# Kernel tuning notes

Measured on AMD Instinct MI355X. Metric: run time of the kernel, lower is better.

## Reference

```python
import jax, jax.numpy as jnp
import numpy as np

NUM_EMBEDDINGS = 8192
EMBEDDING_DIM = 256
COMMITMENT_COST = 0.25


def setup_inputs() -> dict:
    key = jax.random.key(0)
    k1, k2 = jax.random.split(key)
    x = jax.random.normal(k1, (8, 4096, EMBEDDING_DIM), dtype=jnp.float32)
    # torch init: uniform(-1/K, 1/K)
    codebook = jax.random.uniform(
        k2, (NUM_EMBEDDINGS, EMBEDDING_DIM), dtype=jnp.float32,
        minval=-1.0 / NUM_EMBEDDINGS, maxval=1.0 / NUM_EMBEDDINGS)
    return {"x": x, "codebook": codebook}


def reference(x, codebook):
    D = codebook.shape[1]
    K = codebook.shape[0]
    flat_x = x.reshape(-1, D)                      # [N, D]
    distances = (jnp.sum(flat_x * flat_x, axis=1, keepdims=True)
                 + jnp.sum(codebook * codebook, axis=1)
                 - 2.0 * jnp.matmul(flat_x, codebook.T))
    encoding_indices = jnp.argmin(distances, axis=1)  # [N]
    # direct gather instead of one-hot matmul (same math)
    quantized = codebook[encoding_indices].reshape(x.shape)

    sg = jax.lax.stop_gradient
    e_latent_loss = jnp.mean((sg(quantized) - x) ** 2)
    q_latent_loss = jnp.mean((quantized - sg(x)) ** 2)
    loss = q_latent_loss + COMMITMENT_COST * e_latent_loss

    quantized_st = x + sg(quantized - x)

    # avg one-hot probs via counts
    counts = jnp.bincount(encoding_indices, length=K)
    avg_probs = counts.astype(x.dtype) / encoding_indices.shape[0]
    perplexity = jnp.exp(-jnp.sum(avg_probs * jnp.log(avg_probs + 1e-10)))
    return quantized_st, loss, perplexity
```

## Files before the change

kernel.cpp:

```cpp
#include <hip/hip_runtime.h>
#include <cfloat>
#include <math.h>

#define NUM_EMB 8192
#define DIM 256
#define NROWS 32768
#define NSPLIT 4
#define CHUNKS 16

typedef float f32x4 __attribute__((ext_vector_type(4)));
typedef int   i32x4 __attribute__((ext_vector_type(4)));
typedef int   i32x8 __attribute__((ext_vector_type(8)));

#define GL2LDS(g, l) __builtin_amdgcn_global_load_lds( \
    (const __attribute__((address_space(1))) void*)(g), \
    (__attribute__((address_space(3))) void*)(l), 16, 0, 0)

__global__ __launch_bounds__(256) void vq_prep(const float* __restrict__ x,
                                               unsigned char* __restrict__ xq,
                                               const float* __restrict__ cb,
                                               unsigned char* __restrict__ cbq,
                                               float* __restrict__ cbn,
                                               unsigned int* __restrict__ counts) {
    int b = blockIdx.x;
    if (b < 4096) {
        int i = b * 256 + threadIdx.x;
        float4 v0 = ((const float4*)x)[2 * i];
        float4 v1 = ((const float4*)x)[2 * i + 1];
        int p0 = __builtin_amdgcn_cvt_pk_fp8_f32(v0.x, v0.y, 0, false);
        p0     = __builtin_amdgcn_cvt_pk_fp8_f32(v0.z, v0.w, p0, true);
        int p1 = __builtin_amdgcn_cvt_pk_fp8_f32(v1.x, v1.y, 0, false);
        p1     = __builtin_amdgcn_cvt_pk_fp8_f32(v1.z, v1.w, p1, true);
        ((int2*)xq)[i] = make_int2(p0, p1);
    } else if (b < 6144) {
        int row  = (b - 4096) * 4 + (threadIdx.x >> 6);
        int lane = threadIdx.x & 63;
        float4 v = ((const float4*)(cb + (size_t)row * DIM))[lane];
        int p = __builtin_amdgcn_cvt_pk_fp8_f32(v.x * 8192.f, v.y * 8192.f, 0, false);
        p     = __builtin_amdgcn_cvt_pk_fp8_f32(v.z * 8192.f, v.w * 8192.f, p, true);
        ((int*)cbq)[row * 64 + lane] = p;
        float s = v.x * v.x + v.y * v.y + v.z * v.z + v.w * v.w;
        #pragma unroll
        for (int off = 32; off > 0; off >>= 1) s += __shfl_down(s, off, 64);
        if (lane == 0) cbn[row] = 8192.f * s + 512.f;
    } else {
        counts[(b - 6144) * 256 + threadIdx.x] = 0u;
    }
}

__global__ __launch_bounds__(256, 4) void vq_argmin_mfma(
        const unsigned char* __restrict__ xq,
        const unsigned char* __restrict__ cbq,
        const float* __restrict__ cbn,
        unsigned long long* __restrict__ partial) {
    __shared__ __align__(16) unsigned char Bs[128 * 256];
    __shared__ unsigned long long redk[2][64];

    const int tid = threadIdx.x;
    const int lane = tid & 63;
    const int w = tid >> 6;
    const int wm = w >> 1, wn = w & 1;
    const int l15 = lane & 15, q = lane >> 4;
    const int ns = blockIdx.x & (NSPLIT - 1);
    const int by = blockIdx.x / NSPLIT;
    const int m0 = by * 64;
    const int nbase = ns * (NUM_EMB / NSPLIT);

    i32x8 afr[2][2];
    #pragma unroll
    for (int kc = 0; kc < 2; kc++)
        #pragma unroll
        for (int i = 0; i < 2; i++) {
            const unsigned char* p =
                xq + (size_t)(m0 + wm * 32 + i * 16 + l15) * 256 + kc * 128 + q * 32;
            i32x4 lo = *(const i32x4*)p;
            i32x4 hi = *(const i32x4*)(p + 16);
            afr[kc][i] = __builtin_shufflevector(lo, hi, 0, 1, 2, 3, 4, 5, 6, 7);
        }

    unsigned int colb[4];
    #pragma unroll
    for (int j = 0; j < 4; j++) colb[j] = (unsigned)(wn * 64 + j * 16 + l15);

    unsigned int runk[2][4];
    #pragma unroll
    for (int i = 0; i < 2; i++)
        #pragma unroll
        for (int r = 0; r < 4; r++) runk[i][r] = 0xFFFFFFFFu;

    const int sr = lane >> 4;
    const int sv = lane & 15;

    #pragma unroll 1
    for (int ch = 0; ch < CHUNKS; ch++) {
        const int n0c = nbase + ch * 128;
        const unsigned int chb = (unsigned)ch << 7;
        unsigned int cj[4];
        float bnj[4];
        #pragma unroll
        for (int j = 0; j < 4; j++) {
            cj[j] = chb | colb[j];
            bnj[j] = cbn[n0c + (int)colb[j]];
        }

        f32x4 acc[2][4];
        #pragma unroll
        for (int i = 0; i < 2; i++)
            #pragma unroll
            for (int j = 0; j < 4; j++) acc[i][j] = (f32x4)0.f;

        __syncthreads();
        #pragma unroll
        for (int t = 0; t < 8; t++) {
            int s = t * 4 + w;
            int row = s * 4 + sr;
            int kcs = sv >> 3, blk = sv & 7;
            GL2LDS(cbq + (size_t)(n0c + row) * 256 + kcs * 128 + ((blk ^ (row & 7)) * 16),
                   (char*)Bs + s * 1024);
        }
        __syncthreads();

        #pragma unroll
        for (int kc = 0; kc < 2; kc++) {
            #pragma unroll
            for (int j = 0; j < 4; j++) {
                int row = wn * 64 + j * 16 + l15;
                int base = row * 256 + kc * 128;
                int s0 = ((2 * q) ^ (row & 7)) * 16;
                int s1 = ((2 * q + 1) ^ (row & 7)) * 16;
                i32x4 lo = *(const i32x4*)(Bs + base + s0);
                i32x4 hi = *(const i32x4*)(Bs + base + s1);
                i32x8 bfr = __builtin_shufflevector(lo, hi, 0, 1, 2, 3, 4, 5, 6, 7);
                acc[0][j] = __builtin_amdgcn_mfma_scale_f32_16x16x128_f8f6f4(
                    afr[kc][0], bfr, acc[0][j], 0, 0, 0, 127, 0, 127);
                acc[1][j] = __builtin_amdgcn_mfma_scale_f32_16x16x128_f8f6f4(
                    afr[kc][1], bfr, acc[1][j], 0, 0, 0, 127, 0, 127);
            }
        }

        #pragma unroll
        for (int i = 0; i < 2; i++) {
            #pragma unroll
            for (int r = 0; r < 4; r++) {
                unsigned int k0 = (__float_as_uint(fmaf(-2.f, acc[i][0][r], bnj[0])) & 0xFFFFF800u) | cj[0];
                unsigned int k1 = (__float_as_uint(fmaf(-2.f, acc[i][1][r], bnj[1])) & 0xFFFFF800u) | cj[1];
                unsigned int k2 = (__float_as_uint(fmaf(-2.f, acc[i][2][r], bnj[2])) & 0xFFFFF800u) | cj[2];
                unsigned int k3 = (__float_as_uint(fmaf(-2.f, acc[i][3][r], bnj[3])) & 0xFFFFF800u) | cj[3];
                runk[i][r] = min(runk[i][r], min(min(k0, k1), min(k2, k3)));
            }
        }
    }

    #pragma unroll
    for (int i = 0; i < 2; i++) {
        #pragma unroll
        for (int r = 0; r < 4; r++) {
            unsigned int rk = runk[i][r];
            unsigned int gcol = (unsigned)nbase + (rk & 0x7FFu);
            unsigned long long key =
                ((unsigned long long)(rk & 0xFFFFF800u) << 32) | gcol;
            #pragma unroll
            for (int off = 8; off >= 1; off >>= 1) {
                unsigned long long o = __shfl_xor(key, off, 16);
                if (o < key) key = o;
            }
            if (l15 == 0) redk[wn][wm * 32 + i * 16 + q * 4 + r] = key;
        }
    }
    __syncthreads();
    if (tid < 64) {
        unsigned long long k0 = redk[0][tid], k1 = redk[1][tid];
        partial[(size_t)ns * NROWS + m0 + tid] = k0 < k1 ? k0 : k1;
    }
}

__global__ __launch_bounds__(256) void vq_out(const float* __restrict__ x,
                                              const float* __restrict__ cb,
                                              const unsigned long long* __restrict__ partial,
                                              float* __restrict__ out,
                                              unsigned int* __restrict__ counts,
                                              double* __restrict__ loss_part) {
    __shared__ float wred[4];
    int wv   = threadIdx.x >> 6;
    int row  = blockIdx.x * 4 + wv;
    int lane = threadIdx.x & 63;
    unsigned long long k = 0xFFFFFFFFFFFFFFFFull;
    #pragma unroll
    for (int t = 0; t < NSPLIT; t++) {
        unsigned long long v = partial[(size_t)t * NROWS + row];
        if (v < k) k = v;
    }
    int id = (int)(unsigned int)(k & 0xffffffffu);
    float4 qv = ((const float4*)(cb + (size_t)id * DIM))[lane];
    float4 xv = ((const float4*)(x + (size_t)row * DIM))[lane];
    float dx = qv.x - xv.x, dy = qv.y - xv.y, dz = qv.z - xv.z, dw = qv.w - xv.w;
    float4 o;
    o.x = xv.x + dx; o.y = xv.y + dy; o.z = xv.z + dz; o.w = xv.w + dw;
    ((float4*)(out + (size_t)row * DIM))[lane] = o;
    float s = dx * dx + dy * dy + dz * dz + dw * dw;
    #pragma unroll
    for (int o2 = 32; o2 > 0; o2 >>= 1) s += __shfl_down(s, o2, 64);
    if (lane == 0) {
        wred[wv] = s;
        atomicAdd(&counts[id], 1u);
    }
    __syncthreads();
    if (threadIdx.x == 0) {
        loss_part[blockIdx.x] =
            (double)wred[0] + (double)wred[1] + (double)wred[2] + (double)wred[3];
    }
}

__global__ __launch_bounds__(256) void vq_fin(const unsigned int* __restrict__ counts,
                                              const double* __restrict__ loss_part,
                                              float* __restrict__ out_tail) {
    __shared__ double sh[256];
    __shared__ double sl[256];
    int tid = threadIdx.x;
    double h = 0.0;
    for (int k = tid; k < NUM_EMB; k += 256) {
        float p = (float)counts[k] / 32768.0f;
        h += (double)p * log((double)p + 1e-10);
    }
    double ls = 0.0;
    for (int b = tid; b < NROWS / 4; b += 256) ls += loss_part[b];
    sh[tid] = h;
    sl[tid] = ls;
    __syncthreads();
    for (int o = 128; o > 0; o >>= 1) {
        if (tid < o) { sh[tid] += sh[tid + o]; sl[tid] += sl[tid + o]; }
        __syncthreads();
    }
    if (tid == 0) {
        double mean = sl[0] / (double)((size_t)NROWS * DIM);
        out_tail[0] = (float)(1.25 * mean);
        out_tail[1] = (float)exp(-sh[0]);
    }
}

extern "C" void kernel_launch(void* const* d_in, const int* in_sizes, int n_in,
                              void* d_out, int out_size, void* d_ws, size_t ws_size,
                              hipStream_t stream) {
    const float* x  = (const float*)d_in[0];
    const float* cb = (const float*)d_in[1];
    char* ws = (char*)d_ws;
    unsigned int* counts   = (unsigned int*)(ws + 256);
    float* cbn             = (float*)(ws + 33024);
    unsigned char* xq      = (unsigned char*)(ws + 65792);
    unsigned char* cbq     = (unsigned char*)(ws + 65792 + 8388608);
    unsigned long long* pp = (unsigned long long*)(ws + 65792 + 8388608 + 2097152);
    double* loss_part      = (double*)(ws + 65792 + 8388608 + 2097152 + 16777216);
    float* out = (float*)d_out;

    vq_prep       <<<6176, 256, 0, stream>>>(x, xq, cb, cbq, cbn, counts);
    vq_argmin_mfma<<<512 * NSPLIT, 256, 0, stream>>>(xq, cbq, cbn, pp);
    vq_out        <<<8192, 256, 0, stream>>>(x, cb, pp, out, counts, loss_part);
    vq_fin        <<<1, 256, 0, stream>>>(counts, loss_part, out + (size_t)NROWS * DIM);
}
```

Measured before the change: 208.4 us.

## Double-buffer codebook tiles, fold norms into MFMA accumulator, fuse finalize kernel

The argmin kernel now uses 64-column chunks with two LDS buffers, so the next chunk's global-to-LDS loads are issued while the current chunk is computed, and only one barrier is needed per chunk. The input x is negated and the codebook norms are halved, so the MFMA accumulator starts from the norm and the per-element fma is dropped. The separate single-block finalize kernel is folded into vq_out through a last-block ticket counter, removing one launch. This adds atomics and fences for the ticket, and the fast __logf changes entropy precision slightly.

```diff
diff --git a/kernel.cpp b/kernel.cpp
--- a/kernel.cpp
+++ b/kernel.cpp
@@ -6,7 +6,7 @@
 #define DIM 256
 #define NROWS 32768
 #define NSPLIT 4
-#define CHUNKS 16
+#define CHUNKS 32
 
 typedef float f32x4 __attribute__((ext_vector_type(4)));
 typedef int   i32x4 __attribute__((ext_vector_type(4)));
@@ -15,22 +15,26 @@
 #define GL2LDS(g, l) __builtin_amdgcn_global_load_lds( \
     (const __attribute__((address_space(1))) void*)(g), \
     (__attribute__((address_space(3))) void*)(l), 16, 0, 0)
+
+#define MFMA(A, B, C) __builtin_amdgcn_mfma_scale_f32_16x16x128_f8f6f4( \
+    (A), (B), (C), 0, 0, 0, 127, 0, 127)
 
 __global__ __launch_bounds__(256) void vq_prep(const float* __restrict__ x,
                                                unsigned char* __restrict__ xq,
                                                const float* __restrict__ cb,
                                                unsigned char* __restrict__ cbq,
                                                float* __restrict__ cbn,
-                                               unsigned int* __restrict__ counts) {
+                                               unsigned int* __restrict__ counts,
+                                               unsigned int* __restrict__ syncc) {
     int b = blockIdx.x;
     if (b < 4096) {
         int i = b * 256 + threadIdx.x;
         float4 v0 = ((const float4*)x)[2 * i];
         float4 v1 = ((const float4*)x)[2 * i + 1];
-        int p0 = __builtin_amdgcn_cvt_pk_fp8_f32(v0.x, v0.y, 0, false);
-        p0     = __builtin_amdgcn_cvt_pk_fp8_f32(v0.z, v0.w, p0, true);
-        int p1 = __builtin_amdgcn_cvt_pk_fp8_f32(v1.x, v1.y, 0, false);
-        p1     = __builtin_amdgcn_cvt_pk_fp8_f32(v1.z, v1.w, p1, true);
+        int p0 = __builtin_amdgcn_cvt_pk_fp8_f32(-v0.x, -v0.y, 0, false);
+        p0     = __builtin_amdgcn_cvt_pk_fp8_f32(-v0.z, -v0.w, p0, true);
+        int p1 = __builtin_amdgcn_cvt_pk_fp8_f32(-v1.x, -v1.y, 0, false);
+        p1     = __builtin_amdgcn_cvt_pk_fp8_f32(-v1.z, -v1.w, p1, true);
         ((int2*)xq)[i] = make_int2(p0, p1);
     } else if (b < 6144) {
         int row  = (b - 4096) * 4 + (threadIdx.x >> 6);
@@ -42,9 +46,10 @@
         float s = v.x * v.x + v.y * v.y + v.z * v.z + v.w * v.w;
         #pragma unroll
         for (int off = 32; off > 0; off >>= 1) s += __shfl_down(s, off, 64);
-        if (lane == 0) cbn[row] = 8192.f * s + 512.f;
+        if (lane == 0) cbn[row] = 4096.f * s + 256.f;
     } else {
         counts[(b - 6144) * 256 + threadIdx.x] = 0u;
+        if (b == 6144 && threadIdx.x == 0) *syncc = 0u;
     }
 }
 
@@ -53,7 +58,7 @@
         const unsigned char* __restrict__ cbq,
         const float* __restrict__ cbn,
         unsigned long long* __restrict__ partial) {
-    __shared__ __align__(16) unsigned char Bs[128 * 256];
+    __shared__ __align__(16) unsigned char Bs[2][16384];
     __shared__ unsigned long long redk[2][64];
 
     const int tid = threadIdx.x;
@@ -62,25 +67,31 @@
     const int wm = w >> 1, wn = w & 1;
     const int l15 = lane & 15, q = lane >> 4;
     const int ns = blockIdx.x & (NSPLIT - 1);
-    const int by = blockIdx.x / NSPLIT;
+    const int by = blockIdx.x >> 2;
     const int m0 = by * 64;
     const int nbase = ns * (NUM_EMB / NSPLIT);
 
-    i32x8 afr[2][2];
-    #pragma unroll
-    for (int kc = 0; kc < 2; kc++)
-        #pragma unroll
-        for (int i = 0; i < 2; i++) {
-            const unsigned char* p =
-                xq + (size_t)(m0 + wm * 32 + i * 16 + l15) * 256 + kc * 128 + q * 32;
-            i32x4 lo = *(const i32x4*)p;
-            i32x4 hi = *(const i32x4*)(p + 16);
-            afr[kc][i] = __builtin_shufflevector(lo, hi, 0, 1, 2, 3, 4, 5, 6, 7);
-        }
-
-    unsigned int colb[4];
-    #pragma unroll
-    for (int j = 0; j < 4; j++) colb[j] = (unsigned)(wn * 64 + j * 16 + l15);
+    i32x8 afr00, afr01, afr10, afr11;
+    {
+        const unsigned char* p = xq + (size_t)(m0 + wm * 32 + l15) * 256 + q * 32;
+        i32x4 lo, hi;
+        lo = *(const i32x4*)(p);                  hi = *(const i32x4*)(p + 16);
+        afr00 = __builtin_shufflevector(lo, hi, 0, 1, 2, 3, 4, 5, 6, 7);
+        lo = *(const i32x4*)(p + 16 * 256);       hi = *(const i32x4*)(p + 16 * 256 + 16);
+        afr01 = __builtin_shufflevector(lo, hi, 0, 1, 2, 3, 4, 5, 6, 7);
+        lo = *(const i32x4*)(p + 128);            hi = *(const i32x4*)(p + 128 + 16);
+        afr10 = __builtin_shufflevector(lo, hi, 0, 1, 2, 3, 4, 5, 6, 7);
+        lo = *(const i32x4*)(p + 16 * 256 + 128); hi = *(const i32x4*)(p + 16 * 256 + 128 + 16);
+        afr11 = __builtin_shufflevector(lo, hi, 0, 1, 2, 3, 4, 5, 6, 7);
+    }
+
+    const int row0 = wn * 32 + l15;
+    const int sw = row0 & 7;
+    const int vA = row0 * 256 + (((2 * q) ^ sw) * 16);
+    const int vB = row0 * 256 + (((2 * q + 1) ^ sw) * 16);
+
+    const unsigned int colb0 = (unsigned)(wn * 32 + l15);
+    const unsigned int colb1 = colb0 + 16;
 
     unsigned int runk[2][4];
     #pragma unroll
@@ -90,65 +101,74 @@
 
     const int sr = lane >> 4;
     const int sv = lane & 15;
+    const int kcs = sv >> 3, blk = sv & 7;
+    const unsigned char* gs[4];
+    int sg[4];
+    #pragma unroll
+    for (int t = 0; t < 4; t++) {
+        int s = t * 4 + w;
+        int r = s * 4 + sr;
+        gs[t] = cbq + (size_t)(nbase + r) * 256 + (size_t)(kcs * 128 + ((blk ^ (r & 7)) * 16));
+        sg[t] = s * 1024;
+    }
+
+    #pragma unroll
+    for (int t = 0; t < 4; t++) GL2LDS(gs[t], (char*)&Bs[0][0] + sg[t]);
+    #pragma unroll
+    for (int t = 0; t < 4; t++) gs[t] += 16384;
+    const float* bnp = cbn + nbase;
+    float bn0 = bnp[colb0];
+    float bn1 = bnp[colb1];
+    __syncthreads();
+
+#define BLOAD(CUR, OFF) ({ \
+    i32x4 lo_ = *(const i32x4*)(&Bs[CUR][0] + vA + (OFF)); \
+    i32x4 hi_ = *(const i32x4*)(&Bs[CUR][0] + vB + (OFF)); \
+    __builtin_shufflevector(lo_, hi_, 0, 1, 2, 3, 4, 5, 6, 7); })
+
+#define CHUNK_BODY(CHV, CUR, NXT, LAST) do { \
+    float nbn0 = bnp[64 + (int)colb0]; \
+    float nbn1 = bnp[64 + (int)colb1]; \
+    if (!(LAST)) { \
+        GL2LDS(gs[0], (char*)&Bs[NXT][0] + sg[0]); \
+        GL2LDS(gs[1], (char*)&Bs[NXT][0] + sg[1]); \
+        GL2LDS(gs[2], (char*)&Bs[NXT][0] + sg[2]); \
+        GL2LDS(gs[3], (char*)&Bs[NXT][0] + sg[3]); \
+    } \
+    gs[0] += 16384; gs[1] += 16384; gs[2] += 16384; gs[3] += 16384; \
+    f32x4 ci0; ci0[0] = bn0; ci0[1] = bn0; ci0[2] = bn0; ci0[3] = bn0; \
+    f32x4 ci1; ci1[0] = bn1; ci1[1] = bn1; ci1[2] = bn1; ci1[3] = bn1; \
+    i32x8 b_ = BLOAD(CUR, 0); \
+    f32x4 a00 = MFMA(afr00, b_, ci0); \
+    f32x4 a10 = MFMA(afr01, b_, ci0); \
+    b_ = BLOAD(CUR, 128); \
+    a00 = MFMA(afr10, b_, a00); \
+    a10 = MFMA(afr11, b_, a10); \
+    b_ = BLOAD(CUR, 4096); \
+    f32x4 a01 = MFMA(afr00, b_, ci1); \
+    f32x4 a11 = MFMA(afr01, b_, ci1); \
+    b_ = BLOAD(CUR, 4224); \
+    a01 = MFMA(afr10, b_, a01); \
+    a11 = MFMA(afr11, b_, a11); \
+    unsigned int chb = ((unsigned)(CHV)) << 6; \
+    unsigned int cj0 = chb | colb0, cj1 = chb | colb1; \
+    _Pragma("unroll") \
+    for (int r = 0; r < 4; r++) { \
+        unsigned int k00 = (__float_as_uint(a00[r]) & 0xFFFFF800u) | cj0; \
+        unsigned int k01 = (__float_as_uint(a01[r]) & 0xFFFFF800u) | cj1; \
+        runk[0][r] = min(min(k00, k01), runk[0][r]); \
+        unsigned int k10 = (__float_as_uint(a10[r]) & 0xFFFFF800u) | cj0; \
+        unsigned int k11 = (__float_as_uint(a11[r]) & 0xFFFFF800u) | cj1; \
+        runk[1][r] = min(min(k10, k11), runk[1][r]); \
+    } \
+    bn0 = nbn0; bn1 = nbn1; bnp += 64; \
+    __syncthreads(); \
+} while (0)
 
     #pragma unroll 1
-    for (int ch = 0; ch < CHUNKS; ch++) {
-        const int n0c = nbase + ch * 128;
-        const unsigned int chb = (unsigned)ch << 7;
-        unsigned int cj[4];
-        float bnj[4];
-        #pragma unroll
-        for (int j = 0; j < 4; j++) {
-            cj[j] = chb | colb[j];
-            bnj[j] = cbn[n0c + (int)colb[j]];
-        }
-
-        f32x4 acc[2][4];
-        #pragma unroll
-        for (int i = 0; i < 2; i++)
-            #pragma unroll
-            for (int j = 0; j < 4; j++) acc[i][j] = (f32x4)0.f;
-
-        __syncthreads();
-        #pragma unroll
-        for (int t = 0; t < 8; t++) {
-            int s = t * 4 + w;
-            int row = s * 4 + sr;
-            int kcs = sv >> 3, blk = sv & 7;
-            GL2LDS(cbq + (size_t)(n0c + row) * 256 + kcs * 128 + ((blk ^ (row & 7)) * 16),
-                   (char*)Bs + s * 1024);
-        }
-        __syncthreads();
-
-        #pragma unroll
-        for (int kc = 0; kc < 2; kc++) {
-            #pragma unroll
-            for (int j = 0; j < 4; j++) {
-                int row = wn * 64 + j * 16 + l15;
-                int base = row * 256 + kc * 128;
-                int s0 = ((2 * q) ^ (row & 7)) * 16;
-                int s1 = ((2 * q + 1) ^ (row & 7)) * 16;
-                i32x4 lo = *(const i32x4*)(Bs + base + s0);
-                i32x4 hi = *(const i32x4*)(Bs + base + s1);
-                i32x8 bfr = __builtin_shufflevector(lo, hi, 0, 1, 2, 3, 4, 5, 6, 7);
-                acc[0][j] = __builtin_amdgcn_mfma_scale_f32_16x16x128_f8f6f4(
-                    afr[kc][0], bfr, acc[0][j], 0, 0, 0, 127, 0, 127);
-                acc[1][j] = __builtin_amdgcn_mfma_scale_f32_16x16x128_f8f6f4(
-                    afr[kc][1], bfr, acc[1][j], 0, 0, 0, 127, 0, 127);
-            }
-        }
-
-        #pragma unroll
-        for (int i = 0; i < 2; i++) {
-            #pragma unroll
-            for (int r = 0; r < 4; r++) {
-                unsigned int k0 = (__float_as_uint(fmaf(-2.f, acc[i][0][r], bnj[0])) & 0xFFFFF800u) | cj[0];
-                unsigned int k1 = (__float_as_uint(fmaf(-2.f, acc[i][1][r], bnj[1])) & 0xFFFFF800u) | cj[1];
-                unsigned int k2 = (__float_as_uint(fmaf(-2.f, acc[i][2][r], bnj[2])) & 0xFFFFF800u) | cj[2];
-                unsigned int k3 = (__float_as_uint(fmaf(-2.f, acc[i][3][r], bnj[3])) & 0xFFFFF800u) | cj[3];
-                runk[i][r] = min(runk[i][r], min(min(k0, k1), min(k2, k3)));
-            }
-        }
+    for (int ch = 0; ch < CHUNKS; ch += 2) {
+        CHUNK_BODY(ch,     0, 1, false);
+        CHUNK_BODY(ch + 1, 1, 0, (ch + 1) == CHUNKS - 1);
     }
 
     #pragma unroll
@@ -179,11 +199,17 @@
                                               const unsigned long long* __restrict__ partial,
                                               float* __restrict__ out,
                                               unsigned int* __restrict__ counts,
-                                              double* __restrict__ loss_part) {
+                                              double* __restrict__ loss_part,
+                                              unsigned int* __restrict__ syncc,
+                                              float* __restrict__ out_tail) {
     __shared__ float wred[4];
-    int wv   = threadIdx.x >> 6;
-    int row  = blockIdx.x * 4 + wv;
-    int lane = threadIdx.x & 63;
+    __shared__ unsigned int ticket;
+    __shared__ double sh[256];
+    __shared__ double sl[256];
+    const int tid  = threadIdx.x;
+    const int wv   = tid >> 6;
+    const int row  = blockIdx.x * 4 + wv;
+    const int lane = tid & 63;
     unsigned long long k = 0xFFFFFFFFFFFFFFFFull;
     #pragma unroll
     for (int t = 0; t < NSPLIT; t++) {
@@ -205,30 +231,32 @@
         atomicAdd(&counts[id], 1u);
     }
     __syncthreads();
-    if (threadIdx.x == 0) {
+    if (tid == 0) {
         loss_part[blockIdx.x] =
             (double)wred[0] + (double)wred[1] + (double)wred[2] + (double)wred[3];
-    }
-}
-
-__global__ __launch_bounds__(256) void vq_fin(const unsigned int* __restrict__ counts,
-                                              const double* __restrict__ loss_part,
-                                              float* __restrict__ out_tail) {
-    __shared__ double sh[256];
-    __shared__ double sl[256];
-    int tid = threadIdx.x;
-    double h = 0.0;
-    for (int k = tid; k < NUM_EMB; k += 256) {
-        float p = (float)counts[k] / 32768.0f;
-        h += (double)p * log((double)p + 1e-10);
-    }
-    double ls = 0.0;
-    for (int b = tid; b < NROWS / 4; b += 256) ls += loss_part[b];
+        __threadfence();
+        ticket = __hip_atomic_fetch_add(syncc, 1u, __ATOMIC_ACQ_REL,
+                                        __HIP_MEMORY_SCOPE_AGENT);
+    }
+    __syncthreads();
+    if (ticket != (unsigned int)(gridDim.x - 1)) return;
+
+    double h = 0.0, ls = 0.0;
+    for (int kk = tid; kk < NUM_EMB; kk += 256) {
+        unsigned int c = __hip_atomic_load(&counts[kk], __ATOMIC_RELAXED,
+                                           __HIP_MEMORY_SCOPE_AGENT);
+        float p = (float)c * (1.0f / 32768.0f);
+        h += (double)(p * __logf(p + 1e-10f));
+    }
+    for (int bq = tid; bq < NROWS / 4; bq += 256) {
+        ls += __hip_atomic_load(&loss_part[bq], __ATOMIC_RELAXED,
+                                __HIP_MEMORY_SCOPE_AGENT);
+    }
     sh[tid] = h;
     sl[tid] = ls;
     __syncthreads();
-    for (int o = 128; o > 0; o >>= 1) {
-        if (tid < o) { sh[tid] += sh[tid + o]; sl[tid] += sl[tid + o]; }
+    for (int o2 = 128; o2 > 0; o2 >>= 1) {
+        if (tid < o2) { sh[tid] += sh[tid + o2]; sl[tid] += sl[tid + o2]; }
         __syncthreads();
     }
     if (tid == 0) {
@@ -244,6 +272,7 @@
     const float* x  = (const float*)d_in[0];
     const float* cb = (const float*)d_in[1];
     char* ws = (char*)d_ws;
+    unsigned int* syncc    = (unsigned int*)ws;
     unsigned int* counts   = (unsigned int*)(ws + 256);
     float* cbn             = (float*)(ws + 33024);
     unsigned char* xq      = (unsigned char*)(ws + 65792);
@@ -252,8 +281,8 @@
     double* loss_part      = (double*)(ws + 65792 + 8388608 + 2097152 + 16777216);
     float* out = (float*)d_out;
 
-    vq_prep       <<<6176, 256, 0, stream>>>(x, xq, cb, cbq, cbn, counts);
+    vq_prep       <<<6176, 256, 0, stream>>>(x, xq, cb, cbq, cbn, counts, syncc);
     vq_argmin_mfma<<<512 * NSPLIT, 256, 0, stream>>>(xq, cbq, cbn, pp);
-    vq_out        <<<8192, 256, 0, stream>>>(x, cb, pp, out, counts, loss_part);
-    vq_fin        <<<1, 256, 0, stream>>>(counts, loss_part, out + (size_t)NROWS * DIM);
-}
+    vq_out        <<<8192, 256, 0, stream>>>(x, cb, pp, out, counts, loss_part, syncc,
+                                             out + (size_t)NROWS * DIM);
+}
```

Result: slower. 621.6 us (+198.3%).
